# Kernel tuning notes

Hardware: AMD Instinct MI355X
Metric: run time of the kernel (lower is better)

The kernel has to match this reference:

```python
import jax, jax.numpy as jnp
import numpy as np

TOPK = 32

def softsign(x):
    return x / (1.0 + jnp.abs(x))

def setup_inputs() -> dict:
    key = jax.random.key(0)
    k1, k2, k3 = jax.random.split(key, 3)
    B, Q, S, D = 1, 4096, 32768, 256
    return {
        "query_val": jax.random.normal(k1, (B, Q, D), dtype=jnp.float32),
        "source_val": jax.random.normal(k2, (B, S, D), dtype=jnp.float32),
        "source_state": jax.random.normal(k3, (B, S), dtype=jnp.float32),
    }

def reference(query_val, source_val, source_state):
    # pairwise scores (dot-product similarity): [B, Q, S]
    scores = jnp.einsum("bqd,bsd->bqs", query_val, source_val)
    # global top-k over sources == streaming blockwise top-k merge in the original
    top_scores, top_idx = jax.lax.top_k(scores, TOPK)  # [B, Q, K]
    edges = softsign(top_scores)                        # edge_compress_fn
    # gather_state_by_indices: [B, Q, K]
    sel_state = jnp.take_along_axis(source_state[:, None, :], top_idx, axis=-1)
    # gather_val_by_indices: [B, Q, K, D]
    sel_val = jnp.take_along_axis(source_val[:, None, :, :], top_idx[..., None], axis=2)
    delta_state = jnp.sum(edges * sel_state, axis=-1)          # [B, Q]
    delta_val = jnp.sum(edges[..., None] * sel_val, axis=-2)   # [B, Q, D]
    return delta_state, delta_val
```

## Files before the change

### kernel.cpp

```cpp
#include <hip/hip_runtime.h>
#include <stdint.h>

typedef unsigned int u32;
typedef unsigned long long u64;
typedef unsigned short u16;
typedef unsigned char u8;

#define NQ 4096
#define NS 32768
#define ND 256
#define TOPK 32
#define CAP 256
#define CAP2 24
#define ZT 2.75f

#define QB 128
#define SB 32
#define NSLICE 32
#define SLICE (NS / NSLICE)
#define CH (SLICE / SB)

typedef __attribute__((ext_vector_type(8))) __bf16 bf16x8;
typedef __attribute__((ext_vector_type(4))) float f32x4;

#define QB_OFF   (NS * ND * 2)
#define TQ_OFF   (QB_OFF + NQ * ND * 2)
#define C8_OFF   (TQ_OFF + NQ * 4)
#define CD_OFF   (C8_OFF + NQ * NSLICE)

__device__ __forceinline__ u16 f2bf(float x) {
  u32 u = __float_as_uint(x);
  u32 r = u + 0x7FFFu + ((u >> 16) & 1u);
  return (u16)(r >> 16);
}

__global__ void k_prep_src(const float* __restrict__ src, uint4* __restrict__ dst) {
  int t = blockIdx.x * 256 + threadIdx.x;
  const float4* s4 = (const float4*)src + (size_t)t * 2;
  float4 a = s4[0], b = s4[1];
  uint4 o;
  o.x = (u32)f2bf(a.x) | ((u32)f2bf(a.y) << 16);
  o.y = (u32)f2bf(a.z) | ((u32)f2bf(a.w) << 16);
  o.z = (u32)f2bf(b.x) | ((u32)f2bf(b.y) << 16);
  o.w = (u32)f2bf(b.z) | ((u32)f2bf(b.w) << 16);
  dst[t] = o;
}

__global__ void k_prep_q(const float* __restrict__ qv, u16* __restrict__ qb,
                         float* __restrict__ tq) {
  int lane = threadIdx.x & 63, w = threadIdx.x >> 6;
  int q = blockIdx.x * 4 + w;
  float4 v = *((const float4*)(qv + (size_t)q * ND) + lane);
  uint2 p;
  p.x = (u32)f2bf(v.x) | ((u32)f2bf(v.y) << 16);
  p.y = (u32)f2bf(v.z) | ((u32)f2bf(v.w) << 16);
  *((uint2*)(qb + (size_t)q * ND) + lane) = p;
  float s = v.x * v.x + v.y * v.y + v.z * v.z + v.w * v.w;
  #pragma unroll
  for (int o = 1; o < 64; o <<= 1) s += __shfl_xor(s, o, 64);
  if (lane == 0) tq[q] = ZT * sqrtf(s);
}

__global__ __launch_bounds__(256, 4) void k_screen(
    const u16* __restrict__ qb, const u16* __restrict__ srcb,
    const float* __restrict__ tq, u8* __restrict__ cnt8, u32* __restrict__ cand2) {
  __shared__ __align__(16) u16 lds[2][SB * ND];
  __shared__ u32 bcnt[QB];
  const int tid  = threadIdx.x;
  const int lane = tid & 63;
  const int w    = tid >> 6;
  const int l15  = lane & 15, lhi = lane >> 4;

  const int id   = blockIdx.x;
  const int xcd  = id & 7;
  const int rank = id >> 3;
  const int by   = xcd * 4 + (rank >> 5);
  const int bx   = rank & 31;

  const int qbase = bx * QB + w * 32;
  const int sbase = by * SLICE;

  if (tid < QB) bcnt[tid] = 0u;

  bf16x8 afrag[2][8];
  float  thr[2][4];
  #pragma unroll
  for (int mt = 0; mt < 2; ++mt) {
    const u16* qp = qb + (size_t)(qbase + mt * 16 + l15) * ND;
    #pragma unroll
    for (int ks = 0; ks < 8; ++ks)
      afrag[mt][ks] = *((const bf16x8*)(qp + ks * 32 + lhi * 8));
    #pragma unroll
    for (int r = 0; r < 4; ++r) thr[mt][r] = tq[qbase + mt * 16 + lhi * 4 + r];
  }

  int goff[4];
  #pragma unroll
  for (int i = 0; i < 4; ++i) {
    int slot = i * 256 + tid;
    int row  = slot >> 5;
    int o    = (slot & 31) ^ (row & 7);
    goff[i]  = row * ND + o * 8;
  }

#define STAGE(b, c)                                                              \
  {                                                                              \
    const u16* sp_ = srcb + (size_t)(sbase + (c) * SB) * ND;                     \
    _Pragma("unroll")                                                            \
    for (int i_ = 0; i_ < 4; ++i_)                                               \
      __builtin_amdgcn_global_load_lds(                                          \
          (const __attribute__((address_space(1))) void*)(sp_ + goff[i_]),       \
          (__attribute__((address_space(3))) void*)(&lds[b][(i_ * 256 + w * 64) * 8]), \
          16, 0, 0);                                                             \
  }

#define COMPUTE(b, srow0)                                                        \
  {                                                                              \
    f32x4 acc[2][2];                                                             \
    _Pragma("unroll")                                                            \
    for (int mt = 0; mt < 2; ++mt)                                               \
      _Pragma("unroll")                                                          \
      for (int nt = 0; nt < 2; ++nt) acc[mt][nt] = (f32x4){0.f, 0.f, 0.f, 0.f};  \
    _Pragma("unroll")                                                            \
    for (int ks = 0; ks < 8; ++ks) {                                             \
      bf16x8 bfr[2];                                                             \
      _Pragma("unroll")                                                          \
      for (int nt = 0; nt < 2; ++nt) {                                           \
        int r_ = nt * 16 + l15;                                                  \
        int o_ = ks * 4 + lhi;                                                   \
        int slot_ = r_ * 32 + (o_ ^ (r_ & 7));                                   \
        bfr[nt] = *((const bf16x8*)(&lds[b][slot_ * 8]));                        \
      }                                                                          \
      _Pragma("unroll")                                                          \
      for (int mt = 0; mt < 2; ++mt)                                             \
        _Pragma("unroll")                                                        \
        for (int nt = 0; nt < 2; ++nt)                                           \
          acc[mt][nt] = __builtin_amdgcn_mfma_f32_16x16x32_bf16(                 \
              afrag[mt][ks], bfr[nt], acc[mt][nt], 0, 0, 0);                     \
    }                                                                            \
    _Pragma("unroll")                                                            \
    for (int mt = 0; mt < 2; ++mt)                                               \
      _Pragma("unroll")                                                          \
      for (int nt = 0; nt < 2; ++nt)                                             \
        _Pragma("unroll")                                                        \
        for (int r_ = 0; r_ < 4; ++r_) {                                         \
          float sc_ = acc[mt][nt][r_];                                           \
          if (sc_ > thr[mt][r_]) {                                               \
            int ql_ = w * 32 + mt * 16 + lhi * 4 + r_;                           \
            u32 off_ = atomicAdd(&bcnt[ql_], 1u);                                \
            if (off_ < CAP2)                                                     \
              cand2[(((size_t)(qbase + mt * 16 + lhi * 4 + r_)) * NSLICE + by) * CAP2 + off_] = \
                  ((u32)((srow0) + nt * 16 + l15) << 16) | (u32)f2bf(sc_);       \
          }                                                                      \
        }                                                                        \
  }

  STAGE(0, 0);
  __syncthreads();
  int cur = 0;
  for (int c = 0; c < CH - 1; ++c) {
    STAGE(cur ^ 1, c + 1);
    COMPUTE(cur, sbase + c * SB);
    __syncthreads();
    cur ^= 1;
  }
  COMPUTE(cur, sbase + (CH - 1) * SB);
#undef STAGE
#undef COMPUTE

  __syncthreads();
  if (tid < QB) {
    u32 c = bcnt[tid];
    cnt8[(size_t)by * NQ + bx * QB + tid] = (u8)(c < CAP2 ? c : CAP2);
  }
}

__global__ __launch_bounds__(256) void k_finish(
    const float* __restrict__ qval, const float* __restrict__ sval,
    const float* __restrict__ sstate, const u8* __restrict__ cnt8,
    const u32* __restrict__ cand2, float* __restrict__ out) {
  const int q = blockIdx.x;
  const int tid = threadIdx.x;
  const int lane = tid & 63, w = tid >> 6;
  __shared__ u16  scnt[NSLICE];
  __shared__ u16  soff[NSLICE];
  __shared__ u32  skey[CAP];
  __shared__ u32  sidxl[CAP];
  __shared__ u32  ssel[64];
  __shared__ float sexact[64];
  __shared__ u32  ssrc[64];
  __shared__ float fw[TOPK];
  __shared__ u32  fi[TOPK];

  if (tid < NSLICE) scnt[tid] = cnt8[(size_t)tid * NQ + q];
  skey[tid] = 0u;
  __syncthreads();
  if (tid == 0) {
    u32 a = 0;
    #pragma unroll
    for (int s = 0; s < NSLICE; ++s) { soff[s] = (u16)a; a += scnt[s]; }
  }
  __syncthreads();

  {
    int s = tid >> 3, j0 = tid & 7;
    #pragma unroll
    for (int rep = 0; rep < 3; ++rep) {
      int j = j0 + rep * 8;
      if (j < (int)scnt[s]) {
        int p = (int)soff[s] + j;
        if (p < CAP) {
          u32 ent = cand2[((size_t)q * NSLICE + s) * CAP2 + j];
          skey[p]  = ((ent & 0xFFFFu) << 8) | (u32)p;
          sidxl[p] = ent >> 16;
        }
      }
    }
  }
  __syncthreads();

  {
    u32 key = skey[tid];
    #pragma unroll
    for (int k2 = 2; k2 <= 64; k2 <<= 1) {
      #pragma unroll
      for (int j = k2 >> 1; j > 0; j >>= 1) {
        u32 o = __shfl_xor(key, j, 64);
        bool keepMax = ((lane & j) == 0) == ((lane & k2) == 0);
        key = keepMax ? (key > o ? key : o) : (key > o ? o : key);
      }
    }
    skey[tid] = key;
  }
  __syncthreads();

  if (w == 0) {
    u32 a = skey[lane];
    u32 b = skey[64 + (63 ^ lane)];
    u32 m1 = a > b ? a : b;
    u32 c = skey[128 + lane];
    u32 d = skey[192 + (63 ^ lane)];
    u32 m2 = c > d ? c : d;
    #pragma unroll
    for (int j = 32; j > 0; j >>= 1) {
      u32 o1 = __shfl_xor(m1, j, 64);
      m1 = ((lane & j) == 0) ? (m1 > o1 ? m1 : o1) : (m1 > o1 ? o1 : m1);
      u32 o2 = __shfl_xor(m2, j, 64);
      m2 = ((lane & j) == 0) ? (m2 > o2 ? m2 : o2) : (m2 > o2 ? o2 : m2);
    }
    u32 m2r = __shfl(m2, 63 ^ lane, 64);
    ssel[lane] = (m1 > m2r) ? m1 : m2r;
  }
  __syncthreads();

  const int l16 = lane & 15, sub = lane >> 4;
  float4 qf[4];
  #pragma unroll
  for (int j = 0; j < 4; ++j)
    qf[j] = *((const float4*)(qval + (size_t)q * ND) + l16 * 4 + j);
  #pragma unroll
  for (int p = 0; p < 4; ++p) {
    int e = w * 16 + p * 4 + sub;
    u32 key = ssel[e];
    u32 si = sidxl[key & 0xFFu];
    float dp = 0.f;
    if (key) {
      const float4* vp = (const float4*)(sval + (size_t)si * ND) + l16 * 4;
      #pragma unroll
      for (int j = 0; j < 4; ++j) {
        float4 v = vp[j];
        dp += qf[j].x * v.x + qf[j].y * v.y + qf[j].z * v.z + qf[j].w * v.w;
      }
    }
    #pragma unroll
    for (int o = 1; o < 16; o <<= 1) dp += __shfl_xor(dp, o, 64);
    if (l16 == 0) { sexact[e] = key ? dp : -3.0e38f; ssrc[e] = si; }
  }
  __syncthreads();

  if (w == 0) {
    float sc = sexact[lane];
    u32 si  = ssrc[lane];
    u32 kb  = __float_as_uint(sc);
    kb = kb ^ (u32)(((int)kb >> 31) | 0x80000000);
    u64 kk = ((u64)kb << 32) | (u32)(~si);
    #pragma unroll
    for (int k = 2; k <= 64; k <<= 1) {
      #pragma unroll
      for (int j = k >> 1; j > 0; j >>= 1) {
        u64 o = __shfl_xor(kk, j, 64);
        bool keepMax = (((lane & j) == 0) == ((lane & k) == 0));
        kk = keepMax ? (kk > o ? kk : o) : (kk > o ? o : kk);
      }
    }
    u32 si2 = ~((u32)kk);
    u32 kb2 = (u32)(kk >> 32);
    u32 fb  = (kb2 & 0x80000000u) ? (kb2 ^ 0x80000000u) : ~kb2;
    float s = __uint_as_float(fb);
    bool ok = (lane < TOPK) && (s > -1.0e38f);
    float edge = ok ? (s / (1.f + fabsf(s))) : 0.f;
    float contrib = ok ? edge * sstate[si2] : 0.f;
    if (lane < TOPK) { fw[lane] = edge; fi[lane] = ok ? si2 : 0u; }
    #pragma unroll
    for (int o = 1; o < 64; o <<= 1) contrib += __shfl_xor(contrib, o, 64);
    if (lane == 0) out[q] = contrib;
  }
  __syncthreads();

  float acc = 0.f;
  #pragma unroll 8
  for (int k = 0; k < TOPK; ++k)
    acc += fw[k] * sval[(size_t)fi[k] * ND + tid];
  out[NQ + (size_t)q * ND + tid] = acc;
}

extern "C" void kernel_launch(void* const* d_in, const int* in_sizes, int n_in,
                              void* d_out, int out_size, void* d_ws, size_t ws_size,
                              hipStream_t stream) {
  const float* qval   = (const float*)d_in[0];
  const float* sval   = (const float*)d_in[1];
  const float* sstate = (const float*)d_in[2];
  float* out = (float*)d_out;
  char*  ws  = (char*)d_ws;
  u16*   srcb  = (u16*)ws;
  u16*   qbuf  = (u16*)(ws + QB_OFF);
  float* tq    = (float*)(ws + TQ_OFF);
  u8*    cnt8  = (u8*)(ws + C8_OFF);
  u32*   cand2 = (u32*)(ws + CD_OFF);

  k_prep_src<<<(NS * ND / 8) / 256, 256, 0, stream>>>(sval, (uint4*)srcb);
  k_prep_q<<<NQ / 4, 256, 0, stream>>>(qval, qbuf, tq);
  k_screen<<<NQ / QB * NSLICE, 256, 0, stream>>>(qbuf, srcb, tq, cnt8, cand2);
  k_finish<<<NQ, 256, 0, stream>>>(qval, sval, sstate, cnt8, cand2, out);
}
```

Measured before the change: 154.7 us.

## Use 2-wave screen blocks with 64 queries per wave, rework finish gathers

The screen kernel now runs 128 threads per block, with each wave covering 64 query rows (4 M-tiles). Each B fragment loaded from LDS therefore feeds twice as many MFMAs, and setprio is raised around the MFMA bursts. The finish kernel computes each exact dot product with 4 threads per candidate instead of 16, and takes the weighted value sum from the bf16 source copy instead of fp32. This trades more registers and lower occupancy for less LDS traffic, and reduced-precision output values risk exceeding the tolerance.

```diff
diff --git a/kernel.cpp b/kernel.cpp
--- a/kernel.cpp
+++ b/kernel.cpp
@@ -61,7 +61,7 @@
   if (lane == 0) tq[q] = ZT * sqrtf(s);
 }
 
-__global__ __launch_bounds__(256, 4) void k_screen(
+__global__ __launch_bounds__(128, 2) void k_screen(
     const u16* __restrict__ qb, const u16* __restrict__ srcb,
     const float* __restrict__ tq, u8* __restrict__ cnt8, u32* __restrict__ cand2) {
   __shared__ __align__(16) u16 lds[2][SB * ND];
@@ -77,15 +77,15 @@
   const int by   = xcd * 4 + (rank >> 5);
   const int bx   = rank & 31;
 
-  const int qbase = bx * QB + w * 32;
+  const int qbase = bx * QB + w * 64;
   const int sbase = by * SLICE;
 
   if (tid < QB) bcnt[tid] = 0u;
 
-  bf16x8 afrag[2][8];
-  float  thr[2][4];
+  bf16x8 afrag[4][8];
+  float  thr[4][4];
   #pragma unroll
-  for (int mt = 0; mt < 2; ++mt) {
+  for (int mt = 0; mt < 4; ++mt) {
     const u16* qp = qb + (size_t)(qbase + mt * 16 + l15) * ND;
     #pragma unroll
     for (int ks = 0; ks < 8; ++ks)
@@ -94,10 +94,10 @@
     for (int r = 0; r < 4; ++r) thr[mt][r] = tq[qbase + mt * 16 + lhi * 4 + r];
   }
 
-  int goff[4];
+  int goff[8];
   #pragma unroll
-  for (int i = 0; i < 4; ++i) {
-    int slot = i * 256 + tid;
+  for (int i = 0; i < 8; ++i) {
+    int slot = i * 128 + tid;
     int row  = slot >> 5;
     int o    = (slot & 31) ^ (row & 7);
     goff[i]  = row * ND + o * 8;
@@ -107,18 +107,18 @@
   {                                                                              \
     const u16* sp_ = srcb + (size_t)(sbase + (c) * SB) * ND;                     \
     _Pragma("unroll")                                                            \
-    for (int i_ = 0; i_ < 4; ++i_)                                               \
+    for (int i_ = 0; i_ < 8; ++i_)                                               \
       __builtin_amdgcn_global_load_lds(                                          \
           (const __attribute__((address_space(1))) void*)(sp_ + goff[i_]),       \
-          (__attribute__((address_space(3))) void*)(&lds[b][(i_ * 256 + w * 64) * 8]), \
+          (__attribute__((address_space(3))) void*)(&lds[b][(i_ * 128 + w * 64) * 8]), \
           16, 0, 0);                                                             \
   }
 
 #define COMPUTE(b, srow0)                                                        \
   {                                                                              \
-    f32x4 acc[2][2];                                                             \
+    f32x4 acc[4][2];                                                             \
     _Pragma("unroll")                                                            \
-    for (int mt = 0; mt < 2; ++mt)                                               \
+    for (int mt = 0; mt < 4; ++mt)                                               \
       _Pragma("unroll")                                                          \
       for (int nt = 0; nt < 2; ++nt) acc[mt][nt] = (f32x4){0.f, 0.f, 0.f, 0.f};  \
     _Pragma("unroll")                                                            \
@@ -131,22 +131,24 @@
         int slot_ = r_ * 32 + (o_ ^ (r_ & 7));                                   \
         bfr[nt] = *((const bf16x8*)(&lds[b][slot_ * 8]));                        \
       }                                                                          \
+      __builtin_amdgcn_s_setprio(1);                                             \
       _Pragma("unroll")                                                          \
-      for (int mt = 0; mt < 2; ++mt)                                             \
+      for (int mt = 0; mt < 4; ++mt)                                             \
         _Pragma("unroll")                                                        \
         for (int nt = 0; nt < 2; ++nt)                                           \
           acc[mt][nt] = __builtin_amdgcn_mfma_f32_16x16x32_bf16(                 \
               afrag[mt][ks], bfr[nt], acc[mt][nt], 0, 0, 0);                     \
+      __builtin_amdgcn_s_setprio(0);                                             \
     }                                                                            \
     _Pragma("unroll")                                                            \
-    for (int mt = 0; mt < 2; ++mt)                                               \
+    for (int mt = 0; mt < 4; ++mt)                                               \
       _Pragma("unroll")                                                          \
       for (int nt = 0; nt < 2; ++nt)                                             \
         _Pragma("unroll")                                                        \
         for (int r_ = 0; r_ < 4; ++r_) {                                         \
           float sc_ = acc[mt][nt][r_];                                           \
           if (sc_ > thr[mt][r_]) {                                               \
-            int ql_ = w * 32 + mt * 16 + lhi * 4 + r_;                           \
+            int ql_ = w * 64 + mt * 16 + lhi * 4 + r_;                           \
             u32 off_ = atomicAdd(&bcnt[ql_], 1u);                                \
             if (off_ < CAP2)                                                     \
               cand2[(((size_t)(qbase + mt * 16 + lhi * 4 + r_)) * NSLICE + by) * CAP2 + off_] = \
@@ -177,8 +179,9 @@
 
 __global__ __launch_bounds__(256) void k_finish(
     const float* __restrict__ qval, const float* __restrict__ sval,
-    const float* __restrict__ sstate, const u8* __restrict__ cnt8,
-    const u32* __restrict__ cand2, float* __restrict__ out) {
+    const u16* __restrict__ srcb, const float* __restrict__ sstate,
+    const u8* __restrict__ cnt8, const u32* __restrict__ cand2,
+    float* __restrict__ out) {
   const int q = blockIdx.x;
   const int tid = threadIdx.x;
   const int lane = tid & 63, w = tid >> 6;
@@ -253,28 +256,23 @@
   }
   __syncthreads();
 
-  const int l16 = lane & 15, sub = lane >> 4;
-  float4 qf[4];
-  #pragma unroll
-  for (int j = 0; j < 4; ++j)
-    qf[j] = *((const float4*)(qval + (size_t)q * ND) + l16 * 4 + j);
-  #pragma unroll
-  for (int p = 0; p < 4; ++p) {
-    int e = w * 16 + p * 4 + sub;
+  {
+    int e = tid >> 2, qt = tid & 3;
     u32 key = ssel[e];
     u32 si = sidxl[key & 0xFFu];
     float dp = 0.f;
     if (key) {
-      const float4* vp = (const float4*)(sval + (size_t)si * ND) + l16 * 4;
+      const float4* vp = (const float4*)(sval + (size_t)si * ND + qt * 64);
+      const float4* qp = (const float4*)(qval + (size_t)q * ND + qt * 64);
       #pragma unroll
-      for (int j = 0; j < 4; ++j) {
-        float4 v = vp[j];
-        dp += qf[j].x * v.x + qf[j].y * v.y + qf[j].z * v.z + qf[j].w * v.w;
+      for (int j = 0; j < 16; ++j) {
+        float4 v = vp[j], qq = qp[j];
+        dp += qq.x * v.x + qq.y * v.y + qq.z * v.z + qq.w * v.w;
       }
     }
-    #pragma unroll
-    for (int o = 1; o < 16; o <<= 1) dp += __shfl_xor(dp, o, 64);
-    if (l16 == 0) { sexact[e] = key ? dp : -3.0e38f; ssrc[e] = si; }
+    dp += __shfl_xor(dp, 1, 64);
+    dp += __shfl_xor(dp, 2, 64);
+    if (qt == 0) { sexact[e] = key ? dp : -3.0e38f; ssrc[e] = si; }
   }
   __syncthreads();
 
@@ -309,8 +307,10 @@
 
   float acc = 0.f;
   #pragma unroll 8
-  for (int k = 0; k < TOPK; ++k)
-    acc += fw[k] * sval[(size_t)fi[k] * ND + tid];
+  for (int k = 0; k < TOPK; ++k) {
+    u32 b = (u32)srcb[(size_t)fi[k] * ND + tid];
+    acc += fw[k] * __uint_as_float(b << 16);
+  }
   out[NQ + (size_t)q * ND + tid] = acc;
 }
 
@@ -330,6 +330,6 @@
 
   k_prep_src<<<(NS * ND / 8) / 256, 256, 0, stream>>>(sval, (uint4*)srcb);
   k_prep_q<<<NQ / 4, 256, 0, stream>>>(qval, qbuf, tq);
-  k_screen<<<NQ / QB * NSLICE, 256, 0, stream>>>(qbuf, srcb, tq, cnt8, cand2);
-  k_finish<<<NQ, 256, 0, stream>>>(qval, sval, sstate, cnt8, cand2, out);
-}
+  k_screen<<<(NQ / QB) * NSLICE, 128, 0, stream>>>(qbuf, srcb, tq, cnt8, cand2);
+  k_finish<<<NQ, 256, 0, stream>>>(qval, sval, srcb, sstate, cnt8, cand2, out);
+}
```

After: 189.3 us. 22.3% more time.

## Double screen query tile per block and replace wave-level sort with block bitonic sort

Applied to the files above, without the earlier changes.

The screening kernel now processes 256 queries per block, with each wave holding four 16-row query fragments instead of two. This doubles reuse of each staged source tile, halves the number of blocks and lowers the occupancy hint. Separately, the finish kernel's shuffle-based 64-wide sorts plus merge are replaced by a full 256-element block bitonic sort in LDS, with two barriers per step. The larger tile raises register pressure. The new sort adds many syncthreads to a kernel launched once per query.

```diff
diff --git a/kernel.cpp b/kernel.cpp
--- a/kernel.cpp
+++ b/kernel.cpp
@@ -14,7 +14,7 @@
 #define CAP2 24
 #define ZT 2.75f
 
-#define QB 128
+#define QB 256
 #define SB 32
 #define NSLICE 32
 #define SLICE (NS / NSLICE)
@@ -61,7 +61,7 @@
   if (lane == 0) tq[q] = ZT * sqrtf(s);
 }
 
-__global__ __launch_bounds__(256, 4) void k_screen(
+__global__ __launch_bounds__(256, 2) void k_screen(
     const u16* __restrict__ qb, const u16* __restrict__ srcb,
     const float* __restrict__ tq, u8* __restrict__ cnt8, u32* __restrict__ cand2) {
   __shared__ __align__(16) u16 lds[2][SB * ND];
@@ -74,18 +74,18 @@
   const int id   = blockIdx.x;
   const int xcd  = id & 7;
   const int rank = id >> 3;
-  const int by   = xcd * 4 + (rank >> 5);
-  const int bx   = rank & 31;
-
-  const int qbase = bx * QB + w * 32;
+  const int by   = xcd * 4 + (rank >> 4);
+  const int bx   = rank & 15;
+
+  const int qbase = bx * QB + w * 64;
   const int sbase = by * SLICE;
 
-  if (tid < QB) bcnt[tid] = 0u;
-
-  bf16x8 afrag[2][8];
-  float  thr[2][4];
-  #pragma unroll
-  for (int mt = 0; mt < 2; ++mt) {
+  bcnt[tid] = 0u;
+
+  bf16x8 afrag[4][8];
+  float  thr[4][4];
+  #pragma unroll
+  for (int mt = 0; mt < 4; ++mt) {
     const u16* qp = qb + (size_t)(qbase + mt * 16 + l15) * ND;
     #pragma unroll
     for (int ks = 0; ks < 8; ++ks)
@@ -110,15 +110,15 @@
     for (int i_ = 0; i_ < 4; ++i_)                                               \
       __builtin_amdgcn_global_load_lds(                                          \
           (const __attribute__((address_space(1))) void*)(sp_ + goff[i_]),       \
-          (__attribute__((address_space(3))) void*)(&lds[b][(i_ * 256 + w * 64) * 8]), \
+          (__attribute__((address_space(3))) void*)(&lds[b][(i_ * 256 + tid) * 8]), \
           16, 0, 0);                                                             \
   }
 
 #define COMPUTE(b, srow0)                                                        \
   {                                                                              \
-    f32x4 acc[2][2];                                                             \
+    f32x4 acc[4][2];                                                             \
     _Pragma("unroll")                                                            \
-    for (int mt = 0; mt < 2; ++mt)                                               \
+    for (int mt = 0; mt < 4; ++mt)                                               \
       _Pragma("unroll")                                                          \
       for (int nt = 0; nt < 2; ++nt) acc[mt][nt] = (f32x4){0.f, 0.f, 0.f, 0.f};  \
     _Pragma("unroll")                                                            \
@@ -132,21 +132,21 @@
         bfr[nt] = *((const bf16x8*)(&lds[b][slot_ * 8]));                        \
       }                                                                          \
       _Pragma("unroll")                                                          \
-      for (int mt = 0; mt < 2; ++mt)                                             \
+      for (int mt = 0; mt < 4; ++mt)                                             \
         _Pragma("unroll")                                                        \
         for (int nt = 0; nt < 2; ++nt)                                           \
           acc[mt][nt] = __builtin_amdgcn_mfma_f32_16x16x32_bf16(                 \
               afrag[mt][ks], bfr[nt], acc[mt][nt], 0, 0, 0);                     \
     }                                                                            \
     _Pragma("unroll")                                                            \
-    for (int mt = 0; mt < 2; ++mt)                                               \
+    for (int mt = 0; mt < 4; ++mt)                                               \
       _Pragma("unroll")                                                          \
       for (int nt = 0; nt < 2; ++nt)                                             \
         _Pragma("unroll")                                                        \
         for (int r_ = 0; r_ < 4; ++r_) {                                         \
           float sc_ = acc[mt][nt][r_];                                           \
           if (sc_ > thr[mt][r_]) {                                               \
-            int ql_ = w * 32 + mt * 16 + lhi * 4 + r_;                           \
+            int ql_ = w * 64 + mt * 16 + lhi * 4 + r_;                           \
             u32 off_ = atomicAdd(&bcnt[ql_], 1u);                                \
             if (off_ < CAP2)                                                     \
               cand2[(((size_t)(qbase + mt * 16 + lhi * 4 + r_)) * NSLICE + by) * CAP2 + off_] = \
@@ -169,7 +169,7 @@
 #undef COMPUTE
 
   __syncthreads();
-  if (tid < QB) {
+  {
     u32 c = bcnt[tid];
     cnt8[(size_t)by * NQ + bx * QB + tid] = (u8)(c < CAP2 ? c : CAP2);
   }
@@ -186,7 +186,6 @@
   __shared__ u16  soff[NSLICE];
   __shared__ u32  skey[CAP];
   __shared__ u32  sidxl[CAP];
-  __shared__ u32  ssel[64];
   __shared__ float sexact[64];
   __shared__ u32  ssrc[64];
   __shared__ float fw[TOPK];
@@ -219,39 +218,17 @@
   }
   __syncthreads();
 
-  {
-    u32 key = skey[tid];
-    #pragma unroll
-    for (int k2 = 2; k2 <= 64; k2 <<= 1) {
-      #pragma unroll
-      for (int j = k2 >> 1; j > 0; j >>= 1) {
-        u32 o = __shfl_xor(key, j, 64);
-        bool keepMax = ((lane & j) == 0) == ((lane & k2) == 0);
-        key = keepMax ? (key > o ? key : o) : (key > o ? o : key);
-      }
+  for (int k = 2; k <= 256; k <<= 1) {
+    for (int j = k >> 1; j > 0; j >>= 1) {
+      int p = tid ^ j;
+      u32 a = skey[tid], b = skey[p];
+      bool keepMax = ((tid < p) == ((tid & k) == 0));
+      u32 r = keepMax ? (a > b ? a : b) : (a > b ? b : a);
+      __syncthreads();
+      skey[tid] = r;
+      __syncthreads();
     }
-    skey[tid] = key;
-  }
-  __syncthreads();
-
-  if (w == 0) {
-    u32 a = skey[lane];
-    u32 b = skey[64 + (63 ^ lane)];
-    u32 m1 = a > b ? a : b;
-    u32 c = skey[128 + lane];
-    u32 d = skey[192 + (63 ^ lane)];
-    u32 m2 = c > d ? c : d;
-    #pragma unroll
-    for (int j = 32; j > 0; j >>= 1) {
-      u32 o1 = __shfl_xor(m1, j, 64);
-      m1 = ((lane & j) == 0) ? (m1 > o1 ? m1 : o1) : (m1 > o1 ? o1 : m1);
-      u32 o2 = __shfl_xor(m2, j, 64);
-      m2 = ((lane & j) == 0) ? (m2 > o2 ? m2 : o2) : (m2 > o2 ? o2 : m2);
-    }
-    u32 m2r = __shfl(m2, 63 ^ lane, 64);
-    ssel[lane] = (m1 > m2r) ? m1 : m2r;
-  }
-  __syncthreads();
+  }
 
   const int l16 = lane & 15, sub = lane >> 4;
   float4 qf[4];
@@ -261,7 +238,7 @@
   #pragma unroll
   for (int p = 0; p < 4; ++p) {
     int e = w * 16 + p * 4 + sub;
-    u32 key = ssel[e];
+    u32 key = skey[e];
     u32 si = sidxl[key & 0xFFu];
     float dp = 0.f;
     if (key) {
@@ -330,6 +307,6 @@
 
   k_prep_src<<<(NS * ND / 8) / 256, 256, 0, stream>>>(sval, (uint4*)srcb);
   k_prep_q<<<NQ / 4, 256, 0, stream>>>(qval, qbuf, tq);
-  k_screen<<<NQ / QB * NSLICE, 256, 0, stream>>>(qbuf, srcb, tq, cnt8, cand2);
+  k_screen<<<(NQ / QB) * NSLICE, 256, 0, stream>>>(qbuf, srcb, tq, cnt8, cand2);
   k_finish<<<NQ, 256, 0, stream>>>(qval, sval, sstate, cnt8, cand2, out);
 }
```

Result: no change. 153.2 us (-1.0%).
